# Optimization experiments

Measured on AMD Instinct MI355X. Metric: run time of the kernel, lower is better.

The kernel has to match this reference:

```python
import jax, jax.numpy as jnp
import numpy as np

IGNORE_INDEX = 255
LOG_CLAMP = 100.0  # torch BCE clamps log at -100, so -log(x) <= 100


def _neg_log(x, cond):
    # BCE(x, 1) = -log(x), with the torch clamp log(x) >= -100.
    x_safe = jnp.where(cond, jnp.maximum(x, 1e-38), 1.0)
    return jnp.where(cond, jnp.minimum(-jnp.log(x_safe), LOG_CLAMP), 0.0)


def setup_inputs() -> dict:
    key = jax.random.key(0)
    k1, k2 = jax.random.split(key)
    B, C, H, W, D = 1, 20, 256, 256, 32
    pred = jax.random.normal(k1, (B, C, H, W, D), dtype=jnp.float32)
    target = jax.random.randint(k2, (B, H, W, D), 0, C, dtype=jnp.int64)
    return {"pred": pred, "target": target}


def reference(pred, target):
    C = pred.shape[1]
    p = jax.nn.softmax(pred, axis=1)                      # [B,C,H,W,D]
    mask = (target != IGNORE_INDEX)                        # [B,H,W,D]

    # Flatten voxels: [N, C] probs, [N] labels, [N] mask.
    p_flat = jnp.moveaxis(p, 1, -1).reshape(-1, C)
    t_flat = target.reshape(-1)
    m_flat = mask.reshape(-1).astype(p.dtype)
    t_safe = jnp.where(mask.reshape(-1), t_flat, 0).astype(jnp.int32)

    # Per-class reductions in one pass (replaces the per-class python loop):
    # nominator[c] = sum_{masked, t==c} p_c ; ct_count[c] = |{masked, t==c}|
    p_at_t = jnp.take_along_axis(p_flat, t_safe[:, None], axis=1)[:, 0] * m_flat
    nominator = jax.ops.segment_sum(p_at_t, t_safe, num_segments=C)
    ct_count = jax.ops.segment_sum(m_flat, t_safe, num_segments=C)
    sum_p = jnp.einsum('nc,n->c', p_flat, m_flat)          # sum of p_c over masked
    n_masked = jnp.sum(m_flat)

    neg_count = n_masked - ct_count                        # sum(1 - ct)
    spec_num = n_masked - sum_p - ct_count + nominator     # sum((1-p)(1-ct))

    valid = ct_count > 0
    prec = nominator / jnp.maximum(sum_p, 1e-38)
    rec = nominator / jnp.maximum(ct_count, 1.0)
    spec = spec_num / jnp.maximum(neg_count, 1.0)

    loss_c = (_neg_log(prec, valid & (sum_p > 0))
              + _neg_log(rec, valid)
              + _neg_log(spec, valid & (neg_count > 0)))
    count = jnp.sum(valid.astype(p.dtype))
    return jnp.sum(loss_c) / count
```

## Files before the change

### kernel.cpp

```cpp
#include <hip/hip_runtime.h>
#include <math.h>

#define NCLS 20
#define IGNORE_IDX 255
#define LOG2E 1.4426950408889634f
#define NTHR 256
#define NSLOT 32

typedef float v4f __attribute__((ext_vector_type(4)));
typedef int v4i __attribute__((ext_vector_type(4)));

__device__ __forceinline__ float wave_reduce(float v) {
#pragma unroll
  for (int off = 32; off > 0; off >>= 1) v += __shfl_xor(v, off, 64);
  return v;
}

__device__ __forceinline__ float neg_log_clamped(float x, bool cond) {
  if (!cond) return 0.0f;
  float xs = fmaxf(x, 1e-38f);
  return fminf(-logf(xs), 100.0f);
}

__global__ __launch_bounds__(NTHR) void pass1(const float* __restrict__ pred,
                                              const int* __restrict__ target,
                                              float* __restrict__ ws, int N) {
  __shared__ float s_acc[3 * NCLS];
  const int tid = threadIdx.x;
  for (int i = tid; i < 3 * NCLS; i += NTHR) s_acc[i] = 0.0f;
  __syncthreads();

  const int nq = N >> 2;
  const int q = blockIdx.x * NTHR + tid;
  const bool in = (q < nq);

  v4f e[NCLS];
  float w[4] = {0.0f, 0.0f, 0.0f, 0.0f};
  v4f pt = (v4f)(0.0f);
  v4i t4 = {IGNORE_IDX, IGNORE_IDX, IGNORE_IDX, IGNORE_IDX};
#pragma unroll
  for (int c = 0; c < NCLS; ++c) e[c] = (v4f)(0.0f);

  if (in) {
    const int n = q << 2;
    t4 = *reinterpret_cast<const v4i*>(target + n);
    v4f Z = (v4f)(0.0f);
#pragma unroll
    for (int c = 0; c < NCLS; ++c) {
      v4f x = *reinterpret_cast<const v4f*>(pred + (size_t)c * N + n);
#pragma unroll
      for (int j = 0; j < 4; ++j) {
        e[c][j] = __builtin_amdgcn_exp2f(fminf(x[j], 80.0f) * LOG2E);
        Z[j] += e[c][j];
        pt[j] = (c == t4[j]) ? e[c][j] : pt[j];
      }
    }
#pragma unroll
    for (int j = 0; j < 4; ++j) {
      const bool msk = (t4[j] != IGNORE_IDX);
      const float r = __builtin_amdgcn_rcpf(Z[j]);
      w[j] = msk ? r : 0.0f;
    }
  }

#pragma unroll
  for (int c = 0; c < NCLS; ++c) {
    float v = wave_reduce(e[c][0] * w[0] + e[c][1] * w[1] +
                          e[c][2] * w[2] + e[c][3] * w[3]);
    if ((tid & 63) == 0) atomicAdd(&s_acc[c], v);
  }

  if (in) {
#pragma unroll
    for (int j = 0; j < 4; ++j) {
      if (t4[j] != IGNORE_IDX) {
        atomicAdd(&s_acc[NCLS + t4[j]], pt[j] * w[j]);
        atomicAdd(&s_acc[2 * NCLS + t4[j]], 1.0f);
      }
    }
  }
  __syncthreads();

  if (tid < 3 * NCLS)
    atomicAdd(&ws[(size_t)(blockIdx.x & (NSLOT - 1)) * 64 + tid], s_acc[tid]);
}

__global__ __launch_bounds__(64) void pass2(const float* __restrict__ ws,
                                            float* __restrict__ out) {
  __shared__ float s[64];
  const int lane = threadIdx.x;
  float a = 0.0f;
#pragma unroll
  for (int r = 0; r < NSLOT; ++r) a += ws[r * 64 + lane];

  const float n_masked =
      wave_reduce((lane >= 2 * NCLS && lane < 3 * NCLS) ? a : 0.0f);

  s[lane] = a;
  __syncthreads();

  float loss = 0.0f, validf = 0.0f;
  if (lane < NCLS) {
    const float sump = s[lane];
    const float nom = s[NCLS + lane];
    const float cnt = s[2 * NCLS + lane];
    const bool valid = cnt > 0.0f;
    const float prec = nom / fmaxf(sump, 1e-38f);
    const float rec = nom / fmaxf(cnt, 1.0f);
    const float negc = n_masked - cnt;
    const float specn = n_masked - sump - cnt + nom;
    const float spec = specn / fmaxf(negc, 1.0f);
    loss = neg_log_clamped(prec, valid && (sump > 0.0f)) +
           neg_log_clamped(rec, valid) +
           neg_log_clamped(spec, valid && (negc > 0.0f));
    validf = valid ? 1.0f : 0.0f;
  }
  loss = wave_reduce(loss);
  validf = wave_reduce(validf);
  if (lane == 0) out[0] = loss / validf;
}

extern "C" void kernel_launch(void* const* d_in, const int* in_sizes, int n_in,
                              void* d_out, int out_size, void* d_ws, size_t ws_size,
                              hipStream_t stream) {
  const float* pred = (const float*)d_in[0];
  const int* target = (const int*)d_in[1];
  const int N = in_sizes[1];
  const int nq = N >> 2;
  const int nblk = (nq + NTHR - 1) / NTHR;

  hipMemsetAsync(d_ws, 0, NSLOT * 64 * sizeof(float), stream);
  pass1<<<nblk, NTHR, 0, stream>>>(pred, target, (float*)d_ws, N);
  pass2<<<1, 64, 0, stream>>>((const float*)d_ws, (float*)d_out);
}
```

Measured before the change: 253.8 us.

## Switch to scalar per-thread voxel loop with register accumulators and sliced shared atomics

Each thread now processes four voxels strided by the block size, using scalar coalesced loads in place of a float4 load per thread. Per-class probability sums are kept in registers across iterations and flushed once into a 32-way sliced shared-memory array, so the per-voxel wave reductions go away and atomic contention drops. Launch bounds now request higher occupancy. The trade-offs are narrower memory transactions, a serial loop per thread, and an extra per-row reduction over the slices at the end of each block.

Measured after the change: 277.1 us. 9.2% more time.

```diff
diff --git a/kernel.cpp b/kernel.cpp
--- a/kernel.cpp
+++ b/kernel.cpp
@@ -5,10 +5,8 @@
 #define IGNORE_IDX 255
 #define LOG2E 1.4426950408889634f
 #define NTHR 256
+#define VOXPT 4
 #define NSLOT 32
-
-typedef float v4f __attribute__((ext_vector_type(4)));
-typedef int v4i __attribute__((ext_vector_type(4)));
 
 __device__ __forceinline__ float wave_reduce(float v) {
 #pragma unroll
@@ -22,67 +20,61 @@
   return fminf(-logf(xs), 100.0f);
 }
 
-__global__ __launch_bounds__(NTHR) void pass1(const float* __restrict__ pred,
-                                              const int* __restrict__ target,
-                                              float* __restrict__ ws, int N) {
-  __shared__ float s_acc[3 * NCLS];
+__global__ __launch_bounds__(NTHR, 6) void pass1(const float* __restrict__ pred,
+                                                 const int* __restrict__ target,
+                                                 float* __restrict__ ws, int N) {
+  __shared__ float s_acc[3 * NCLS][32];
   const int tid = threadIdx.x;
-  for (int i = tid; i < 3 * NCLS; i += NTHR) s_acc[i] = 0.0f;
+  const int sl = tid & 31;
+
+  {
+    float* p = &s_acc[0][0];
+    for (int i = tid; i < 3 * NCLS * 32; i += NTHR) p[i] = 0.0f;
+  }
   __syncthreads();
 
-  const int nq = N >> 2;
-  const int q = blockIdx.x * NTHR + tid;
-  const bool in = (q < nq);
+  float accp[NCLS];
+#pragma unroll
+  for (int c = 0; c < NCLS; ++c) accp[c] = 0.0f;
 
-  v4f e[NCLS];
-  float w[4] = {0.0f, 0.0f, 0.0f, 0.0f};
-  v4f pt = (v4f)(0.0f);
-  v4i t4 = {IGNORE_IDX, IGNORE_IDX, IGNORE_IDX, IGNORE_IDX};
+  const int base = blockIdx.x * (NTHR * VOXPT);
+#pragma unroll 1
+  for (int it = 0; it < VOXPT; ++it) {
+    const int n = base + it * NTHR + tid;
+    if (n < N) {
+      const int t = target[n];
+      float e[NCLS];
+      float Z = 0.0f;
+      float pt = 0.0f;
 #pragma unroll
-  for (int c = 0; c < NCLS; ++c) e[c] = (v4f)(0.0f);
-
-  if (in) {
-    const int n = q << 2;
-    t4 = *reinterpret_cast<const v4i*>(target + n);
-    v4f Z = (v4f)(0.0f);
+      for (int c = 0; c < NCLS; ++c) {
+        const float x = pred[(size_t)c * N + n];
+        e[c] = __builtin_amdgcn_exp2f(fminf(x, 80.0f) * LOG2E);
+        Z += e[c];
+        pt = (c == t) ? e[c] : pt;
+      }
+      const bool msk = (t != IGNORE_IDX);
+      const float w = msk ? __builtin_amdgcn_rcpf(Z) : 0.0f;
 #pragma unroll
-    for (int c = 0; c < NCLS; ++c) {
-      v4f x = *reinterpret_cast<const v4f*>(pred + (size_t)c * N + n);
-#pragma unroll
-      for (int j = 0; j < 4; ++j) {
-        e[c][j] = __builtin_amdgcn_exp2f(fminf(x[j], 80.0f) * LOG2E);
-        Z[j] += e[c][j];
-        pt[j] = (c == t4[j]) ? e[c][j] : pt[j];
+      for (int c = 0; c < NCLS; ++c) accp[c] += e[c] * w;
+      if (msk) {
+        atomicAdd(&s_acc[NCLS + t][sl], pt * w);
+        atomicAdd(&s_acc[2 * NCLS + t][sl], 1.0f);
       }
-    }
-#pragma unroll
-    for (int j = 0; j < 4; ++j) {
-      const bool msk = (t4[j] != IGNORE_IDX);
-      const float r = __builtin_amdgcn_rcpf(Z[j]);
-      w[j] = msk ? r : 0.0f;
     }
   }
 
 #pragma unroll
-  for (int c = 0; c < NCLS; ++c) {
-    float v = wave_reduce(e[c][0] * w[0] + e[c][1] * w[1] +
-                          e[c][2] * w[2] + e[c][3] * w[3]);
-    if ((tid & 63) == 0) atomicAdd(&s_acc[c], v);
-  }
-
-  if (in) {
-#pragma unroll
-    for (int j = 0; j < 4; ++j) {
-      if (t4[j] != IGNORE_IDX) {
-        atomicAdd(&s_acc[NCLS + t4[j]], pt[j] * w[j]);
-        atomicAdd(&s_acc[2 * NCLS + t4[j]], 1.0f);
-      }
-    }
-  }
+  for (int c = 0; c < NCLS; ++c) atomicAdd(&s_acc[c][sl], accp[c]);
   __syncthreads();
 
-  if (tid < 3 * NCLS)
-    atomicAdd(&ws[(size_t)(blockIdx.x & (NSLOT - 1)) * 64 + tid], s_acc[tid]);
+  if (tid < 3 * NCLS) {
+    const float* row = s_acc[tid];
+    float v = 0.0f;
+#pragma unroll
+    for (int i = 0; i < 32; ++i) v += row[(i + tid) & 31];
+    atomicAdd(&ws[(size_t)(blockIdx.x & (NSLOT - 1)) * 64 + tid], v);
+  }
 }
 
 __global__ __launch_bounds__(64) void pass2(const float* __restrict__ ws,
@@ -126,8 +118,8 @@
   const float* pred = (const float*)d_in[0];
   const int* target = (const int*)d_in[1];
   const int N = in_sizes[1];
-  const int nq = N >> 2;
-  const int nblk = (nq + NTHR - 1) / NTHR;
+  const int per_blk = NTHR * VOXPT;
+  const int nblk = (N + per_blk - 1) / per_blk;
 
   hipMemsetAsync(d_ws, 0, NSLOT * 64 * sizeof(float), stream);
   pass1<<<nblk, NTHR, 0, stream>>>(pred, target, (float*)d_ws, N);
```

## Recompute exponentials in second pass and use 32-way privatized LDS accumulators

Applied to the files above, without the earlier changes.

Drops the 80-register per-thread array of exponentials by re-reading pred and recomputing exp2 after the normalizer is known, which lowers register pressure. The 20 per-class wave shuffle reductions are replaced with LDS atomics into 32 lane-privatized slots per accumulator, summed at block end with a rotated index. This trades a second read of pred (likely served from cache) and extra exp work for higher occupancy and no cross-lane shuffles. LDS atomics into the slots still conflict, since lanes 32 apart share a slot.

Result: slower. 294.8 us (+16.2%).

```diff
diff --git a/kernel.cpp b/kernel.cpp
--- a/kernel.cpp
+++ b/kernel.cpp
@@ -25,64 +25,69 @@
 __global__ __launch_bounds__(NTHR) void pass1(const float* __restrict__ pred,
                                               const int* __restrict__ target,
                                               float* __restrict__ ws, int N) {
-  __shared__ float s_acc[3 * NCLS];
+  __shared__ float s_acc[3 * NCLS][32];
   const int tid = threadIdx.x;
-  for (int i = tid; i < 3 * NCLS; i += NTHR) s_acc[i] = 0.0f;
+  const int sl = tid & 31;
+
+  {
+    float* p = &s_acc[0][0];
+    for (int i = tid; i < 3 * NCLS * 32; i += NTHR) p[i] = 0.0f;
+  }
   __syncthreads();
 
   const int nq = N >> 2;
   const int q = blockIdx.x * NTHR + tid;
-  const bool in = (q < nq);
 
-  v4f e[NCLS];
-  float w[4] = {0.0f, 0.0f, 0.0f, 0.0f};
-  v4f pt = (v4f)(0.0f);
-  v4i t4 = {IGNORE_IDX, IGNORE_IDX, IGNORE_IDX, IGNORE_IDX};
-#pragma unroll
-  for (int c = 0; c < NCLS; ++c) e[c] = (v4f)(0.0f);
+  if (q < nq) {
+    const int n = q << 2;
+    const v4i t4 = *reinterpret_cast<const v4i*>(target + n);
 
-  if (in) {
-    const int n = q << 2;
-    t4 = *reinterpret_cast<const v4i*>(target + n);
     v4f Z = (v4f)(0.0f);
+    v4f pt = (v4f)(0.0f);
 #pragma unroll
     for (int c = 0; c < NCLS; ++c) {
-      v4f x = *reinterpret_cast<const v4f*>(pred + (size_t)c * N + n);
+      const v4f x = *reinterpret_cast<const v4f*>(pred + (size_t)c * N + n);
 #pragma unroll
       for (int j = 0; j < 4; ++j) {
-        e[c][j] = __builtin_amdgcn_exp2f(fminf(x[j], 80.0f) * LOG2E);
-        Z[j] += e[c][j];
-        pt[j] = (c == t4[j]) ? e[c][j] : pt[j];
+        const float e = __builtin_amdgcn_exp2f(fminf(x[j], 80.0f) * LOG2E);
+        Z[j] += e;
+        pt[j] = (c == t4[j]) ? e : pt[j];
       }
+    }
+
+    v4f w;
+#pragma unroll
+    for (int j = 0; j < 4; ++j) {
+      const bool msk = (t4[j] != IGNORE_IDX);
+      w[j] = msk ? __builtin_amdgcn_rcpf(Z[j]) : 0.0f;
     }
 #pragma unroll
     for (int j = 0; j < 4; ++j) {
-      const bool msk = (t4[j] != IGNORE_IDX);
-      const float r = __builtin_amdgcn_rcpf(Z[j]);
-      w[j] = msk ? r : 0.0f;
+      if (t4[j] != IGNORE_IDX) {
+        atomicAdd(&s_acc[NCLS + t4[j]][sl], pt[j] * w[j]);
+        atomicAdd(&s_acc[2 * NCLS + t4[j]][sl], 1.0f);
+      }
     }
-  }
 
 #pragma unroll
-  for (int c = 0; c < NCLS; ++c) {
-    float v = wave_reduce(e[c][0] * w[0] + e[c][1] * w[1] +
-                          e[c][2] * w[2] + e[c][3] * w[3]);
-    if ((tid & 63) == 0) atomicAdd(&s_acc[c], v);
-  }
-
-  if (in) {
+    for (int c = 0; c < NCLS; ++c) {
+      const v4f x = *reinterpret_cast<const v4f*>(pred + (size_t)c * N + n);
+      float v = 0.0f;
 #pragma unroll
-    for (int j = 0; j < 4; ++j) {
-      if (t4[j] != IGNORE_IDX) {
-        atomicAdd(&s_acc[NCLS + t4[j]], pt[j] * w[j]);
-        atomicAdd(&s_acc[2 * NCLS + t4[j]], 1.0f);
-      }
+      for (int j = 0; j < 4; ++j)
+        v += __builtin_amdgcn_exp2f(fminf(x[j], 80.0f) * LOG2E) * w[j];
+      atomicAdd(&s_acc[c][sl], v);
     }
   }
   __syncthreads();
 
-  if (tid < 3 * NCLS)
-    atomicAdd(&ws[(size_t)(blockIdx.x & (NSLOT - 1)) * 64 + tid], s_acc[tid]);
+  if (tid < 3 * NCLS) {
+    const float* row = s_acc[tid];
+    float v = 0.0f;
+#pragma unroll
+    for (int i = 0; i < 32; ++i) v += row[(i + tid) & 31];
+    atomicAdd(&ws[(size_t)(blockIdx.x & (NSLOT - 1)) * 64 + tid], v);
+  }
 }
 
 __global__ __launch_bounds__(64) void pass2(const float* __restrict__ ws,
```

## Privatize shared-memory class accumulators into 32 lane slots and use nontemporal loads

Applied to the files above, without the earlier changes.

Replaces the per-class wave shuffle reductions and the single-slot shared atomics with 32-way privatized shared accumulators indexed by lane, so atomics from different lanes hit different banks. The final per-class sum walks the 32 slots with a rotated index to avoid bank conflicts. It also marks the streaming pred loads as nontemporal to reduce cache pollution. The trade-off is more shared memory per block and more shared atomics, since every thread now issues 20 atomics instead of one lane per wave.

After: 280.2 us. +10.4%, slower.

```diff
diff --git a/kernel.cpp b/kernel.cpp
--- a/kernel.cpp
+++ b/kernel.cpp
@@ -25,9 +25,14 @@
 __global__ __launch_bounds__(NTHR) void pass1(const float* __restrict__ pred,
                                               const int* __restrict__ target,
                                               float* __restrict__ ws, int N) {
-  __shared__ float s_acc[3 * NCLS];
+  __shared__ float s_acc[3 * NCLS][32];
   const int tid = threadIdx.x;
-  for (int i = tid; i < 3 * NCLS; i += NTHR) s_acc[i] = 0.0f;
+  const int sl = tid & 31;
+
+  {
+    float* p = &s_acc[0][0];
+    for (int i = tid; i < 3 * NCLS * 32; i += NTHR) p[i] = 0.0f;
+  }
   __syncthreads();
 
   const int nq = N >> 2;
@@ -47,7 +52,8 @@
     v4f Z = (v4f)(0.0f);
 #pragma unroll
     for (int c = 0; c < NCLS; ++c) {
-      v4f x = *reinterpret_cast<const v4f*>(pred + (size_t)c * N + n);
+      const v4f x = __builtin_nontemporal_load(
+          reinterpret_cast<const v4f*>(pred + (size_t)c * N + n));
 #pragma unroll
       for (int j = 0; j < 4; ++j) {
         e[c][j] = __builtin_amdgcn_exp2f(fminf(x[j], 80.0f) * LOG2E);
@@ -65,24 +71,29 @@
 
 #pragma unroll
   for (int c = 0; c < NCLS; ++c) {
-    float v = wave_reduce(e[c][0] * w[0] + e[c][1] * w[1] +
-                          e[c][2] * w[2] + e[c][3] * w[3]);
-    if ((tid & 63) == 0) atomicAdd(&s_acc[c], v);
+    const float s = e[c][0] * w[0] + e[c][1] * w[1] +
+                    e[c][2] * w[2] + e[c][3] * w[3];
+    atomicAdd(&s_acc[c][sl], s);
   }
 
   if (in) {
 #pragma unroll
     for (int j = 0; j < 4; ++j) {
       if (t4[j] != IGNORE_IDX) {
-        atomicAdd(&s_acc[NCLS + t4[j]], pt[j] * w[j]);
-        atomicAdd(&s_acc[2 * NCLS + t4[j]], 1.0f);
+        atomicAdd(&s_acc[NCLS + t4[j]][sl], pt[j] * w[j]);
+        atomicAdd(&s_acc[2 * NCLS + t4[j]][sl], 1.0f);
       }
     }
   }
   __syncthreads();
 
-  if (tid < 3 * NCLS)
-    atomicAdd(&ws[(size_t)(blockIdx.x & (NSLOT - 1)) * 64 + tid], s_acc[tid]);
+  if (tid < 3 * NCLS) {
+    const float* row = s_acc[tid];
+    float v = 0.0f;
+#pragma unroll
+    for (int i = 0; i < 32; ++i) v += row[(i + tid) & 31];
+    atomicAdd(&ws[(size_t)(blockIdx.x & (NSLOT - 1)) * 64 + tid], v);
+  }
 }
 
 __global__ __launch_bounds__(64) void pass2(const float* __restrict__ ws,
```
